# Kernel optimization log

Hardware: AMD Instinct MI355X
Metric: run time of the kernel (lower is better)

Reference implementation:

```python
import jax, jax.numpy as jnp
import numpy as np

NF4 = jnp.array([-1.0, -0.6961928009986877, -0.5250730514526367, -0.39491748809814453,
                 -0.28444138169288635, -0.18477343022823334, -0.09105003625154495, 0.0,
                 0.07958029955625534, 0.16093020141124725, 0.24611230194568634,
                 0.33791524171829224, 0.44070982933044434, 0.5626170039176941,
                 0.7229568362236023, 1.0], dtype=jnp.float32)
BLOCK_SIZE = 64
SCALING = 32.0 / 16.0  # alpha / rank


def setup_inputs() -> dict:
    key = jax.random.key(0)
    k = jax.random.split(key, 6)
    B, S, IN, OUT, R = 4, 128, 4096, 11008, 16
    n_blocks = (OUT * IN) // BLOCK_SIZE  # 704512, exact (no padding needed)
    return {
        "x": jax.random.normal(k[0], (B, S, IN), jnp.float32),
        "weight_indices": jax.random.randint(k[1], (OUT, IN), 0, 16, dtype=jnp.int32),
        "weight_scales": jax.random.uniform(k[2], (n_blocks,), jnp.float32),
        "lora_A": jax.random.normal(k[3], (IN, R), jnp.float32),
        "lora_B": jax.random.normal(k[4], (R, OUT), jnp.float32),
        "bias": jax.random.normal(k[5], (OUT,), jnp.float32),
    }


def dequantize_nf4(indices, scales, shape):
    # LUT gather then blockwise absmax scale
    w = NF4[indices.reshape(-1)]                    # [out*in]
    w = w.reshape(-1, BLOCK_SIZE) * scales[:, None]  # [n_blocks, block]
    return w.reshape(shape)                          # [out, in]


def reference(x, weight_indices, weight_scales, lora_A, lora_B, bias):
    W = dequantize_nf4(weight_indices, weight_scales, weight_indices.shape)  # [out, in]
    base = jnp.einsum("bsi,oi->bso", x, W) + bias                            # F.linear
    lora = (x @ lora_A) @ lora_B                                             # low-rank path (dropout p=0 -> identity)
    return base + lora * SCALING
```

## Files before the change

### kernel.cpp

```cpp
#include <hip/hip_runtime.h>
#include <stdint.h>

typedef __bf16 bf16x8 __attribute__((ext_vector_type(8)));
typedef float f32x4 __attribute__((ext_vector_type(4)));
typedef unsigned short ushort_t;

#define N_OUT 11008
#define K_DIM 4096
#define M_DIM 512
#define BM 128
#define BN 64
#define BK 64
#define NT 64
#define LDB 72
#define BUF (64 * LDB)

__constant__ float c_nf4[16] = {
    -1.0f, -0.6961928009986877f, -0.5250730514526367f, -0.39491748809814453f,
    -0.28444138169288635f, -0.18477343022823334f, -0.09105003625154495f, 0.0f,
    0.07958029955625534f, 0.16093020141124725f, 0.24611230194568634f,
    0.33791524171829224f, 0.44070982933044434f, 0.5626170039176941f,
    0.7229568362236023f, 1.0f};

__device__ __forceinline__ uint32_t pkbf(float lo, float hi) {
  uint32_t ul = __builtin_bit_cast(uint32_t, lo);
  uint32_t uh = __builtin_bit_cast(uint32_t, hi);
  return ((ul + 0x8000u) >> 16) | ((uh + 0x8000u) & 0xffff0000u);
}

__device__ __forceinline__ bf16x8 ldfrag(const ushort_t* p) {
  uint4 r = *reinterpret_cast<const uint4*>(p);
  return __builtin_bit_cast(bf16x8, r);
}

__device__ __forceinline__ bf16x8 asfrag(uint4 r) {
  return __builtin_bit_cast(bf16x8, r);
}

struct DQTab {
  uint32_t thi[4], tlo[4];
};

__device__ __forceinline__ DQTab build_tab(const float* fl, float s) {
  DQTab t;
  uint32_t p[8];
#pragma unroll
  for (int j = 0; j < 8; ++j) p[j] = pkbf(fl[2 * j] * s, fl[2 * j + 1] * s);
#pragma unroll
  for (int j = 0; j < 4; ++j) {
    t.thi[j] = __builtin_amdgcn_perm(p[2 * j + 1], p[2 * j], 0x07050301u);
    t.tlo[j] = __builtin_amdgcn_perm(p[2 * j + 1], p[2 * j], 0x06040200u);
  }
  return t;
}

__device__ __forceinline__ uint32_t pack4(int4 v) {
  return (uint32_t)v.x | ((uint32_t)v.y << 8) | ((uint32_t)v.z << 16) |
         ((uint32_t)v.w << 24);
}

__device__ __forceinline__ uint2 lookup4(uint32_t X, const DQTab& t) {
  uint32_t selA = X & 0x07070707u;
  uint32_t m = X & 0x08080808u;
  uint32_t bsel = 0x03020100u + (m >> 1);
  uint32_t hA = __builtin_amdgcn_perm(t.thi[1], t.thi[0], selA);
  uint32_t hB = __builtin_amdgcn_perm(t.thi[3], t.thi[2], selA);
  uint32_t H = __builtin_amdgcn_perm(hB, hA, bsel);
  uint32_t lA = __builtin_amdgcn_perm(t.tlo[1], t.tlo[0], selA);
  uint32_t lB = __builtin_amdgcn_perm(t.tlo[3], t.tlo[2], selA);
  uint32_t L = __builtin_amdgcn_perm(lB, lA, bsel);
  uint2 r;
  r.x = __builtin_amdgcn_perm(H, L, 0x05010400u);
  r.y = __builtin_amdgcn_perm(H, L, 0x07030602u);
  return r;
}

__global__ void k_prep(const float* __restrict__ x, const float* __restrict__ lA,
                       const float* __restrict__ lB, ushort_t* __restrict__ xbf,
                       ushort_t* __restrict__ xap, ushort_t* __restrict__ btp) {
  __shared__ float red[16][17];
  const int b = blockIdx.x, t = threadIdx.x;
  if (b < 1024) {
    int oc = b * 256 + t;
    const float4* s4 = reinterpret_cast<const float4*>(x) + (size_t)oc * 2;
    float4 v0 = s4[0], v1 = s4[1];
    uint4 o;
    o.x = pkbf(v0.x, v0.y);
    o.y = pkbf(v0.z, v0.w);
    o.z = pkbf(v1.x, v1.y);
    o.w = pkbf(v1.z, v1.w);
    ((uint4*)xbf)[oc] = o;
  } else if (b < 1536) {
    int m = b - 1024;
    int r = t & 15, part = t >> 4;
    const float* xr = x + (size_t)m * K_DIM + part * 256;
    const float* ar = lA + (size_t)(part * 256) * 16 + r;
    float acc = 0.f;
#pragma unroll 8
    for (int k = 0; k < 256; ++k) acc += xr[k] * ar[(size_t)k * 16];
    red[part][r] = acc;
    __syncthreads();
    if (t < 32) {
      float v = 0.f;
      if (t < 16) {
        for (int p = 0; p < 16; ++p) v += red[p][t];
        v *= 2.0f;
      }
      uint32_t u = __builtin_bit_cast(uint32_t, v);
      xap[(size_t)m * 32 + t] = (ushort_t)((u + 0x8000u) >> 16);
    }
  } else {
    int o = (b - 1536) * 256 + t;
    uint32_t p[8];
#pragma unroll
    for (int j = 0; j < 8; ++j)
      p[j] = pkbf(lB[(size_t)(2 * j) * N_OUT + o], lB[(size_t)(2 * j + 1) * N_OUT + o]);
    uint4* dst = reinterpret_cast<uint4*>(btp + (size_t)o * 32);
    dst[0] = make_uint4(p[0], p[1], p[2], p[3]);
    dst[1] = make_uint4(p[4], p[5], p[6], p[7]);
    dst[2] = make_uint4(0u, 0u, 0u, 0u);
    dst[3] = make_uint4(0u, 0u, 0u, 0u);
  }
}

__launch_bounds__(256, 3)
__global__ void k_main(const ushort_t* __restrict__ xbf, const int* __restrict__ wi,
                       const float* __restrict__ sc, const ushort_t* __restrict__ xap,
                       const ushort_t* __restrict__ btp, const float* __restrict__ bias,
                       float* __restrict__ out) {
  __shared__ __align__(16) ushort_t lds_b[2 * BUF];

  const int b = blockIdx.x;
  const int xcd = b & 7, sl = b >> 3;
  const int o_idx = xcd * 22 + (sl >> 2);
  if (o_idx >= 172) return;
  const int m0 = (sl & 3) * BM;
  const int o0 = o_idx * BN;

  const int t = threadIdx.x;
  const int lane = t & 63;
  const int w = t >> 6;
  const int q = lane >> 4;

  float fl[16];
#pragma unroll
  for (int i = 0; i < 16; ++i) fl[i] = c_nf4[i];

  const int brow = t >> 2, bq = t & 3;
  const int* gb = wi + (size_t)(o0 + brow) * K_DIM + bq * 16;
  const float* gs = sc + (size_t)(o0 + brow) * 64;
  const int lbo = brow * LDB + bq * 16;

  const ushort_t* gA = xbf + (size_t)(m0 + w * 32 + (lane & 15)) * K_DIM + q * 8;

  f32x4 acc[2][4];
#pragma unroll
  for (int mi = 0; mi < 2; ++mi)
#pragma unroll
    for (int ni = 0; ni < 4; ++ni) acc[mi][ni] = (f32x4){0.f, 0.f, 0.f, 0.f};

  int4 bi[2][4];
  float bs2[2];
  uint4 a_reg[2][2];
  int4 b0[4];
#pragma unroll
  for (int j = 0; j < 4; ++j) b0[j] = reinterpret_cast<const int4*>(gb)[j];
  float s0 = gs[0];
#pragma unroll
  for (int j = 0; j < 4; ++j) bi[1][j] = reinterpret_cast<const int4*>(gb + 64)[j];
  bs2[1] = gs[1];
#pragma unroll
  for (int j = 0; j < 4; ++j) bi[0][j] = reinterpret_cast<const int4*>(gb + 128)[j];
  bs2[0] = gs[2];
#pragma unroll
  for (int mi = 0; mi < 2; ++mi)
#pragma unroll
    for (int kc = 0; kc < 2; ++kc)
      a_reg[mi][kc] =
          *reinterpret_cast<const uint4*>(gA + (size_t)mi * 16 * K_DIM + kc * 32);

  {
    DQTab tb = build_tab(fl, s0);
    uint2 w0 = lookup4(pack4(b0[0]), tb);
    uint2 w1 = lookup4(pack4(b0[1]), tb);
    uint2 w2 = lookup4(pack4(b0[2]), tb);
    uint2 w3 = lookup4(pack4(b0[3]), tb);
    ushort_t* lb = lds_b + lbo;
    *reinterpret_cast<uint4*>(lb) = make_uint4(w0.x, w0.y, w1.x, w1.y);
    *reinterpret_cast<uint4*>(lb + 8) = make_uint4(w2.x, w2.y, w3.x, w3.y);
  }

#pragma unroll 2
  for (int kt = 0; kt < NT; ++kt) {
    __syncthreads();
    const ushort_t* bb = lds_b + (kt & 1) * BUF + (lane & 15) * LDB + q * 8;
    const int ns = (kt + 1) & 1;
    if (kt + 1 < NT) {
      DQTab tb = build_tab(fl, bs2[ns]);
      uint2 w0 = lookup4(pack4(bi[ns][0]), tb);
      uint2 w1 = lookup4(pack4(bi[ns][1]), tb);
      uint2 w2 = lookup4(pack4(bi[ns][2]), tb);
      uint2 w3 = lookup4(pack4(bi[ns][3]), tb);
      ushort_t* lb = lds_b + ns * BUF + lbo;
      *reinterpret_cast<uint4*>(lb) = make_uint4(w0.x, w0.y, w1.x, w1.y);
      *reinterpret_cast<uint4*>(lb + 8) = make_uint4(w2.x, w2.y, w3.x, w3.y);
    }
    {
      bf16x8 bv[4];
#pragma unroll
      for (int ni = 0; ni < 4; ++ni) bv[ni] = ldfrag(bb + ni * 16 * LDB);
#pragma unroll
      for (int mi = 0; mi < 2; ++mi)
#pragma unroll
        for (int ni = 0; ni < 4; ++ni)
          acc[mi][ni] = __builtin_amdgcn_mfma_f32_16x16x32_bf16(
              asfrag(a_reg[mi][0]), bv[ni], acc[mi][ni], 0, 0, 0);
    }
    {
      bf16x8 bv[4];
#pragma unroll
      for (int ni = 0; ni < 4; ++ni) bv[ni] = ldfrag(bb + ni * 16 * LDB + 32);
#pragma unroll
      for (int mi = 0; mi < 2; ++mi)
#pragma unroll
        for (int ni = 0; ni < 4; ++ni)
          acc[mi][ni] = __builtin_amdgcn_mfma_f32_16x16x32_bf16(
              asfrag(a_reg[mi][1]), bv[ni], acc[mi][ni], 0, 0, 0);
    }
    if (kt + 3 < NT) {
      const int4* gp = reinterpret_cast<const int4*>(gb + (size_t)(kt + 3) * 64);
#pragma unroll
      for (int j = 0; j < 4; ++j) bi[ns][j] = gp[j];
      bs2[ns] = gs[kt + 3];
    }
    if (kt + 1 < NT) {
#pragma unroll
      for (int mi = 0; mi < 2; ++mi)
#pragma unroll
        for (int kc = 0; kc < 2; ++kc)
          a_reg[mi][kc] = *reinterpret_cast<const uint4*>(
              gA + (size_t)mi * 16 * K_DIM + (size_t)(kt + 1) * 64 + kc * 32);
    }
  }

  {
    uint4 la[2], lb4[4];
#pragma unroll
    for (int mi = 0; mi < 2; ++mi)
      la[mi] = *reinterpret_cast<const uint4*>(
          xap + (size_t)(m0 + w * 32 + mi * 16 + (lane & 15)) * 32 + q * 8);
#pragma unroll
    for (int ni = 0; ni < 4; ++ni)
      lb4[ni] = *reinterpret_cast<const uint4*>(
          btp + (size_t)(o0 + ni * 16 + (lane & 15)) * 32 + q * 8);
#pragma unroll
    for (int mi = 0; mi < 2; ++mi)
#pragma unroll
      for (int ni = 0; ni < 4; ++ni)
        acc[mi][ni] = __builtin_amdgcn_mfma_f32_16x16x32_bf16(
            asfrag(la[mi]), asfrag(lb4[ni]), acc[mi][ni], 0, 0, 0);
  }

  const int cl = lane & 15, rg = q * 4;
#pragma unroll
  for (int ni = 0; ni < 4; ++ni) {
    int col = o0 + ni * 16 + cl;
    float bvs = bias[col];
#pragma unroll
    for (int mi = 0; mi < 2; ++mi) {
      int row0 = m0 + w * 32 + mi * 16 + rg;
      float* op = out + (size_t)row0 * N_OUT + col;
#pragma unroll
      for (int i = 0; i < 4; ++i) op[(size_t)i * N_OUT] = acc[mi][ni][i] + bvs;
    }
  }
}

extern "C" void kernel_launch(void* const* d_in, const int* in_sizes, int n_in,
                              void* d_out, int out_size, void* d_ws, size_t ws_size,
                              hipStream_t stream) {
  const float* x = (const float*)d_in[0];
  const int* wi = (const int*)d_in[1];
  const float* sc = (const float*)d_in[2];
  const float* lA = (const float*)d_in[3];
  const float* lB = (const float*)d_in[4];
  const float* bias = (const float*)d_in[5];
  float* out = (float*)d_out;

  char* wsb = (char*)d_ws;
  ushort_t* xbf = (ushort_t*)wsb;
  ushort_t* xap = (ushort_t*)(wsb + (4u << 20));
  ushort_t* btp = (ushort_t*)(wsb + (4u << 20) + (32u << 10));

  k_prep<<<1579, 256, 0, stream>>>(x, lA, lB, xbf, xap, btp);
  k_main<<<704, 256, 0, stream>>>(xbf, wi, sc, xap, btp, bias, out);
}
```

Baseline: 391.4 us.

## Restructure k-loop prefetch: packed index registers and double-buffered A fragments

Reworks the main-loop software pipeline. Weight indices are now packed to bytes right after loading, so only 4 registers are held instead of two sets of 16. A fragments are double-buffered and issued at the top of each iteration, ahead of the dequantize and MFMA work. Index loads move from a three-tile to a two-tile lookahead, which trades some latency hiding on the weight stream for lower register pressure and earlier A loads. Scales rotate through two scalar registers.

```diff
diff --git a/kernel.cpp b/kernel.cpp
--- a/kernel.cpp
+++ b/kernel.cpp
@@ -73,6 +73,17 @@
   r.x = __builtin_amdgcn_perm(H, L, 0x05010400u);
   r.y = __builtin_amdgcn_perm(H, L, 0x07030602u);
   return r;
+}
+
+__device__ __forceinline__ void dq_store(const uint32_t* pi, float s,
+                                         const float* fl, ushort_t* lb) {
+  DQTab tb = build_tab(fl, s);
+  uint2 w0 = lookup4(pi[0], tb);
+  uint2 w1 = lookup4(pi[1], tb);
+  uint2 w2 = lookup4(pi[2], tb);
+  uint2 w3 = lookup4(pi[3], tb);
+  *reinterpret_cast<uint4*>(lb) = make_uint4(w0.x, w0.y, w1.x, w1.y);
+  *reinterpret_cast<uint4*>(lb + 8) = make_uint4(w2.x, w2.y, w3.x, w3.y);
 }
 
 __global__ void k_prep(const float* __restrict__ x, const float* __restrict__ lA,
@@ -128,7 +139,7 @@
                        const float* __restrict__ sc, const ushort_t* __restrict__ xap,
                        const ushort_t* __restrict__ btp, const float* __restrict__ bias,
                        float* __restrict__ out) {
-  __shared__ __align__(16) ushort_t lds_b[2 * BUF];
+  __shared__ __align__(16) ushort_t lds_w[2 * BUF];
 
   const int b = blockIdx.x;
   const int xcd = b & 7, sl = b >> 3;
@@ -159,52 +170,50 @@
 #pragma unroll
     for (int ni = 0; ni < 4; ++ni) acc[mi][ni] = (f32x4){0.f, 0.f, 0.f, 0.f};
 
-  int4 bi[2][4];
-  float bs2[2];
-  uint4 a_reg[2][2];
-  int4 b0[4];
-#pragma unroll
-  for (int j = 0; j < 4; ++j) b0[j] = reinterpret_cast<const int4*>(gb)[j];
-  float s0 = gs[0];
-#pragma unroll
-  for (int j = 0; j < 4; ++j) bi[1][j] = reinterpret_cast<const int4*>(gb + 64)[j];
-  bs2[1] = gs[1];
-#pragma unroll
-  for (int j = 0; j < 4; ++j) bi[0][j] = reinterpret_cast<const int4*>(gb + 128)[j];
-  bs2[0] = gs[2];
+  uint32_t pi[4];
+  {
+    uint32_t p0[4];
+#pragma unroll
+    for (int j = 0; j < 4; ++j) p0[j] = pack4(reinterpret_cast<const int4*>(gb)[j]);
+    dq_store(p0, gs[0], fl, lds_w + lbo);
+  }
+#pragma unroll
+  for (int j = 0; j < 4; ++j) pi[j] = pack4(reinterpret_cast<const int4*>(gb + 64)[j]);
+  float s_have = gs[1], s_next = gs[2];
+
+  uint4 a_reg[2][2][2];
 #pragma unroll
   for (int mi = 0; mi < 2; ++mi)
 #pragma unroll
     for (int kc = 0; kc < 2; ++kc)
-      a_reg[mi][kc] =
+      a_reg[0][mi][kc] =
           *reinterpret_cast<const uint4*>(gA + (size_t)mi * 16 * K_DIM + kc * 32);
-
-  {
-    DQTab tb = build_tab(fl, s0);
-    uint2 w0 = lookup4(pack4(b0[0]), tb);
-    uint2 w1 = lookup4(pack4(b0[1]), tb);
-    uint2 w2 = lookup4(pack4(b0[2]), tb);
-    uint2 w3 = lookup4(pack4(b0[3]), tb);
-    ushort_t* lb = lds_b + lbo;
-    *reinterpret_cast<uint4*>(lb) = make_uint4(w0.x, w0.y, w1.x, w1.y);
-    *reinterpret_cast<uint4*>(lb + 8) = make_uint4(w2.x, w2.y, w3.x, w3.y);
-  }
 
 #pragma unroll 2
   for (int kt = 0; kt < NT; ++kt) {
     __syncthreads();
-    const ushort_t* bb = lds_b + (kt & 1) * BUF + (lane & 15) * LDB + q * 8;
-    const int ns = (kt + 1) & 1;
+    const int cur = kt & 1, ns = cur ^ 1;
+
     if (kt + 1 < NT) {
-      DQTab tb = build_tab(fl, bs2[ns]);
-      uint2 w0 = lookup4(pack4(bi[ns][0]), tb);
-      uint2 w1 = lookup4(pack4(bi[ns][1]), tb);
-      uint2 w2 = lookup4(pack4(bi[ns][2]), tb);
-      uint2 w3 = lookup4(pack4(bi[ns][3]), tb);
-      ushort_t* lb = lds_b + ns * BUF + lbo;
-      *reinterpret_cast<uint4*>(lb) = make_uint4(w0.x, w0.y, w1.x, w1.y);
-      *reinterpret_cast<uint4*>(lb + 8) = make_uint4(w2.x, w2.y, w3.x, w3.y);
-    }
+#pragma unroll
+      for (int mi = 0; mi < 2; ++mi)
+#pragma unroll
+        for (int kc = 0; kc < 2; ++kc)
+          a_reg[ns][mi][kc] = *reinterpret_cast<const uint4*>(
+              gA + (size_t)mi * 16 * K_DIM + (size_t)(kt + 1) * 64 + kc * 32);
+    }
+    int4 ri[4];
+    const bool ld = (kt + 2 < NT);
+    if (ld) {
+      const int4* gp = reinterpret_cast<const int4*>(gb + (size_t)(kt + 2) * 64);
+#pragma unroll
+      for (int j = 0; j < 4; ++j) ri[j] = gp[j];
+    }
+    float snew = (kt + 3 < NT) ? gs[kt + 3] : 0.f;
+
+    if (kt + 1 < NT) dq_store(pi, s_have, fl, lds_w + ns * BUF + lbo);
+
+    const ushort_t* bb = lds_w + cur * BUF + (lane & 15) * LDB + q * 8;
     {
       bf16x8 bv[4];
 #pragma unroll
@@ -214,7 +223,7 @@
 #pragma unroll
         for (int ni = 0; ni < 4; ++ni)
           acc[mi][ni] = __builtin_amdgcn_mfma_f32_16x16x32_bf16(
-              asfrag(a_reg[mi][0]), bv[ni], acc[mi][ni], 0, 0, 0);
+              asfrag(a_reg[cur][mi][0]), bv[ni], acc[mi][ni], 0, 0, 0);
     }
     {
       bf16x8 bv[4];
@@ -225,22 +234,15 @@
 #pragma unroll
         for (int ni = 0; ni < 4; ++ni)
           acc[mi][ni] = __builtin_amdgcn_mfma_f32_16x16x32_bf16(
-              asfrag(a_reg[mi][1]), bv[ni], acc[mi][ni], 0, 0, 0);
-    }
-    if (kt + 3 < NT) {
-      const int4* gp = reinterpret_cast<const int4*>(gb + (size_t)(kt + 3) * 64);
-#pragma unroll
-      for (int j = 0; j < 4; ++j) bi[ns][j] = gp[j];
-      bs2[ns] = gs[kt + 3];
-    }
-    if (kt + 1 < NT) {
-#pragma unroll
-      for (int mi = 0; mi < 2; ++mi)
-#pragma unroll
-        for (int kc = 0; kc < 2; ++kc)
-          a_reg[mi][kc] = *reinterpret_cast<const uint4*>(
-              gA + (size_t)mi * 16 * K_DIM + (size_t)(kt + 1) * 64 + kc * 32);
-    }
+              asfrag(a_reg[cur][mi][1]), bv[ni], acc[mi][ni], 0, 0, 0);
+    }
+
+    if (ld) {
+#pragma unroll
+      for (int j = 0; j < 4; ++j) pi[j] = pack4(ri[j]);
+    }
+    s_have = s_next;
+    s_next = snew;
   }
 
   {
```

Measured after the change: 390.1 us. No clear change (-0.3%).
